# Performance work log

Hardware: AMD Instinct MI355X
Metric: run time of the kernel (lower is better)

Reference implementation:

```python
import jax, jax.numpy as jnp
import numpy as np

TAU = 2.0
V_TH = 1.0
SG_ALPHA = 4.0  # spikingjelly default sigmoid surrogate alpha
BN_EPS = 1e-5

@jax.custom_vjp
def spike_fn(v):
    return (v >= V_TH).astype(v.dtype)

def _spike_fwd(v):
    return spike_fn(v), v

def _spike_bwd(v, g):
    s = jax.nn.sigmoid(SG_ALPHA * (v - V_TH))
    return (g * SG_ALPHA * s * (1.0 - s),)

spike_fn.defvjp(_spike_fwd, _spike_bwd)

def lif(x):
    """Multi-step LIF, tau=2, hard reset to 0, detach_reset. x: (T, ...)."""
    def step(v, xt):
        v = v + (xt - v) / TAU
        s = spike_fn(v)
        v = v * (1.0 - jax.lax.stop_gradient(s))
        return v, s
    _, spikes = jax.lax.scan(step, jnp.zeros_like(x[0]), x)
    return spikes

def batchnorm1d(x, gamma, beta):
    """Training-mode BatchNorm1d over channel dim. x: (N, C, L)."""
    mean = jnp.mean(x, axis=(0, 2), keepdims=True)
    var = jnp.var(x, axis=(0, 2), keepdims=True)  # biased, as torch uses for normalization
    xhat = (x - mean) * jax.lax.rsqrt(var + BN_EPS)
    return xhat * gamma[None, :, None] + beta[None, :, None]

def setup_inputs() -> dict:
    key = jax.random.key(0)
    k_x, k_w1, k_w2 = jax.random.split(key, 3)
    T, B, L, D, H = 4, 64, 64, 768, 3072
    x = jax.random.normal(k_x, (T, B, L, D), dtype=jnp.float32)
    W1 = jax.random.normal(k_w1, (H, D), dtype=jnp.float32) / np.sqrt(D)
    gamma1 = jnp.ones((H,), dtype=jnp.float32)
    beta1 = jnp.zeros((H,), dtype=jnp.float32)
    W2 = jax.random.normal(k_w2, (D, H), dtype=jnp.float32) / np.sqrt(H)
    gamma2 = jnp.ones((D,), dtype=jnp.float32)
    beta2 = jnp.zeros((D,), dtype=jnp.float32)
    return {"x": x, "W1": W1, "gamma1": gamma1, "beta1": beta1,
            "W2": W2, "gamma2": gamma2, "beta2": beta2}

def reference(x, W1, gamma1, beta1, W2, gamma2, beta2):
    T, B, L, D = x.shape
    H = W1.shape[0]
    # --- block 1 ---
    s = lif(x)                                        # (T,B,L,D)
    h = jnp.einsum('tbld,hd->tblh', s, W1)            # (T,B,L,H)
    h = batchnorm1d(h.reshape(T * B, L, H).transpose(0, 2, 1), gamma1, beta1)  # (T*B,H,L)
    # faithful quirk: reshape WITHOUT transposing back
    h = h.reshape(T, B, L, H)
    # --- block 2 ---
    s2 = lif(h)                                       # (T,B,L,H)
    o = jnp.einsum('tblh,dh->tbld', s2, W2)           # (T,B,L,D)
    o = batchnorm1d(o.reshape(T * B, L, D).transpose(0, 2, 1), gamma2, beta2)  # (T*B,D,L)
    o = o.reshape(T, B, L, D)
    return o
```

## Files before the change

kernel.cpp:

```cpp
#include <hip/hip_runtime.h>
#include <stdint.h>
#include <stddef.h>

#define T_ 4
#define B_ 64
#define L_ 64
#define D_ 768
#define H_ 3072
#define M1_ 16384
#define BLD_ 3145728
#define NW_ 2359296
#define HL_ 196608

using f4    = __attribute__((ext_vector_type(4))) float;
using int4v = __attribute__((ext_vector_type(4))) int;
using uc4   = __attribute__((ext_vector_type(4))) unsigned char;
using uc16  = __attribute__((ext_vector_type(16))) unsigned char;
using ui2   = __attribute__((ext_vector_type(2))) unsigned int;

static __device__ __forceinline__ void gload_lds16(const void* g, void* l) {
  __builtin_amdgcn_global_load_lds((const __attribute__((address_space(1))) void*)g,
                                   (__attribute__((address_space(3))) void*)l, 16, 0, 0);
}

#define INV33 (1.0/8589934592.0)

__global__ __launch_bounds__(256) void k_convert(
    const float* __restrict__ W1, const float* __restrict__ W2,
    signed char* __restrict__ Q0, signed char* __restrict__ Q1,
    signed char* __restrict__ Q2, signed char* __restrict__ Q3,
    int* __restrict__ Qint,
    signed char* __restrict__ R0, signed char* __restrict__ R1) {
  int i = blockIdx.x * 256 + threadIdx.x;
  if (i >= NW_) return;
  {
    double w = (double)W1[i];
    long long q = llrint(w * 8589934592.0);
    if (q >  2113929216LL) q =  2113929216LL;
    if (q < -2113929216LL) q = -2113929216LL;
    int ii = (int)q;
    Qint[i] = ii;
    int b0 = ((ii + 128) & 255) - 128; ii = (ii - b0) >> 8;
    int b1 = ((ii + 128) & 255) - 128; ii = (ii - b1) >> 8;
    int b2 = ((ii + 128) & 255) - 128; ii = (ii - b2) >> 8;
    Q0[i] = (signed char)b0; Q1[i] = (signed char)b1;
    Q2[i] = (signed char)b2; Q3[i] = (signed char)ii;
  }
  {
    double w = (double)W2[i];
    long long q = llrint(w * 131072.0);
    if (q >  32512LL) q =  32512LL;
    if (q < -32512LL) q = -32512LL;
    int ii = (int)q;
    int b0 = ((ii + 128) & 255) - 128;
    R0[i] = (signed char)b0;
    R1[i] = (signed char)((ii - b0) >> 8);
  }
}

__global__ __launch_bounds__(256) void k_lif1(const float* __restrict__ x,
                                              unsigned char* __restrict__ s1) {
  size_t i = ((size_t)blockIdx.x * 256 + threadIdx.x) * 4;
  double v0 = 0., v1 = 0., v2 = 0., v3 = 0.;
  #pragma unroll
  for (int t = 0; t < T_; ++t) {
    f4 xt = *(const f4*)(x + (size_t)t * BLD_ + i);
    v0 = v0 + ((double)xt.x - v0) * 0.5;
    v1 = v1 + ((double)xt.y - v1) * 0.5;
    v2 = v2 + ((double)xt.z - v2) * 0.5;
    v3 = v3 + ((double)xt.w - v3) * 0.5;
    uc4 s;
    s.x = (v0 >= 1.0) ? 1 : 0;
    s.y = (v1 >= 1.0) ? 1 : 0;
    s.z = (v2 >= 1.0) ? 1 : 0;
    s.w = (v3 >= 1.0) ? 1 : 0;
    *(uc4*)(s1 + (size_t)t * BLD_ + i) = s;
    v0 = s.x ? 0. : v0;
    v1 = s.y ? 0. : v1;
    v2 = s.z ? 0. : v2;
    v3 = s.w ? 0. : v3;
  }
}

__global__ __launch_bounds__(256) void k_s1t(const unsigned char* __restrict__ s1,
                                             unsigned char* __restrict__ sT,
                                             int* __restrict__ colsum) {
  __shared__ __align__(16) unsigned char sm[64 * 80];
  const int tid = threadIdx.x;
  const int d0 = blockIdx.x * 64;
  const int bl0 = blockIdx.y * 64;
  const int t = blockIdx.z;
  {
    const int i = tid >> 2, ch = tid & 3;
    uc16 v = *(const uc16*)(s1 + (size_t)t * BLD_ + (size_t)(bl0 + i) * 768 + d0 + ch * 16);
    *(uc16*)(sm + i * 80 + ch * 16) = v;
  }
  __syncthreads();
  {
    const int d = tid >> 2, oc = tid & 3;
    union { uc16 v; unsigned char b[16]; } u;
    int s = 0;
    #pragma unroll
    for (int jj = 0; jj < 16; ++jj) {
      unsigned char c = sm[(oc * 16 + jj) * 80 + d];
      u.b[jj] = c;
      s += c;
    }
    *(uc16*)(sT + (size_t)(d0 + d) * M1_ + t * 4096 + bl0 + oc * 16) = u.v;
    s += __shfl_xor(s, 1);
    s += __shfl_xor(s, 2);
    if ((tid & 3) == 0) atomicAdd(&colsum[d0 + d], s);
  }
}

__global__ __launch_bounds__(256, 2) void k_gram(const unsigned char* __restrict__ sT,
                                                 int* __restrict__ Gpart) {
  __shared__ __align__(16) char smem[32768];
  const int tid = threadIdx.x;
  const int lane = tid & 63;
  const int wr = tid >> 7;
  const int wc = (tid >> 6) & 1;
  const int tr = blockIdx.x / 6, tc = blockIdx.x % 6;
  const int ks = blockIdx.y;
  const size_t m0 = (size_t)ks * 2048;

  const int s0 = tid, s1i = tid + 256;
  const int rA0 = s0 >> 2, rA1 = s1i >> 2;
  const int cA0 = (s0 & 3) ^ ((rA0 >> 1) & 3);
  const int cA1 = (s1i & 3) ^ ((rA1 >> 1) & 3);
  const unsigned char* Ag0 = sT + (size_t)(tr * 128 + rA0) * M1_ + m0 + cA0 * 16;
  const unsigned char* Ag1 = sT + (size_t)(tr * 128 + rA1) * M1_ + m0 + cA1 * 16;
  const unsigned char* Bg0 = sT + (size_t)(tc * 128 + rA0) * M1_ + m0 + cA0 * 16;
  const unsigned char* Bg1 = sT + (size_t)(tc * 128 + rA1) * M1_ + m0 + cA1 * 16;

  int4v acc[4][4] = {};
  const int clog = lane >> 4;

  gload_lds16(Ag0, smem + s0 * 16);
  gload_lds16(Ag1, smem + s1i * 16);
  gload_lds16(Bg0, smem + 8192 + s0 * 16);
  gload_lds16(Bg1, smem + 8192 + s1i * 16);
  __syncthreads();

  for (int kt = 0; kt < 32; ++kt) {
    if (kt < 31) {
      const int kn = (kt + 1) * 64;
      char* dst = smem + ((kt + 1) & 1) * 16384;
      gload_lds16(Ag0 + kn, dst + s0 * 16);
      gload_lds16(Ag1 + kn, dst + s1i * 16);
      gload_lds16(Bg0 + kn, dst + 8192 + s0 * 16);
      gload_lds16(Bg1 + kn, dst + 8192 + s1i * 16);
    }
    const signed char* ldsA = (const signed char*)smem + (kt & 1) * 16384;
    const signed char* ldsB = ldsA + 8192;
    int4v av[4], bv[4];
    #pragma unroll
    for (int m = 0; m < 4; ++m) {
      const int r = wr * 64 + m * 16 + (lane & 15);
      const int cp = clog ^ ((r >> 1) & 3);
      av[m] = *(const int4v*)(ldsA + r * 64 + cp * 16);
    }
    #pragma unroll
    for (int n = 0; n < 4; ++n) {
      const int r = wc * 64 + n * 16 + (lane & 15);
      const int cp = clog ^ ((r >> 1) & 3);
      bv[n] = *(const int4v*)(ldsB + r * 64 + cp * 16);
    }
    #pragma unroll
    for (int m = 0; m < 4; ++m)
      #pragma unroll
      for (int n = 0; n < 4; ++n)
        acc[m][n] = __builtin_amdgcn_mfma_i32_16x16x64_i8(av[m], bv[n], acc[m][n], 0, 0, 0);
    __syncthreads();
  }

  const int r0 = tr * 128 + wr * 64 + (clog << 2);
  const int c0 = tc * 128 + wc * 64 + (lane & 15);
  #pragma unroll
  for (int m = 0; m < 4; ++m)
    #pragma unroll
    for (int n = 0; n < 4; ++n)
      #pragma unroll
      for (int rr = 0; rr < 4; ++rr)
        Gpart[((size_t)ks * 768 + r0 + m * 16 + rr) * 768 + c0 + n * 16] = acc[m][n][rr];
}

__global__ __launch_bounds__(256) void k_gramred(const int* __restrict__ Gpart,
                                                 signed char* __restrict__ g0,
                                                 signed char* __restrict__ g1) {
  int i = blockIdx.x * 256 + threadIdx.x;
  if (i >= 768 * 768) return;
  int G = 0;
  #pragma unroll
  for (int ks = 0; ks < 8; ++ks) G += Gpart[(size_t)ks * 768 * 768 + i];
  int b0 = ((G + 128) & 255) - 128;
  g0[i] = (signed char)b0;
  g1[i] = (signed char)((G - b0) >> 8);
}

__global__ __launch_bounds__(256, 2) void k_gq(
    const signed char* __restrict__ g0, const signed char* __restrict__ g1,
    const signed char* __restrict__ Q0, const signed char* __restrict__ Q1,
    const signed char* __restrict__ Q2, const signed char* __restrict__ Q3,
    double* __restrict__ YT) {
  __shared__ __align__(16) char smem[49152];
  const int tid = threadIdx.x;
  const int lane = tid & 63;
  const int w = tid >> 6;
  const int k0 = blockIdx.x * 64;
  const int c0 = blockIdx.y * 64;

  const int row = tid >> 2;
  const int ch = (tid & 3) ^ ((row >> 1) & 3);
  const signed char* Ag[2] = { g0 + (size_t)(k0 + row) * 768 + ch * 16,
                               g1 + (size_t)(k0 + row) * 768 + ch * 16 };
  const signed char* Bg[4] = { Q0 + (size_t)(c0 + row) * 768 + ch * 16,
                               Q1 + (size_t)(c0 + row) * 768 + ch * 16,
                               Q2 + (size_t)(c0 + row) * 768 + ch * 16,
                               Q3 + (size_t)(c0 + row) * 768 + ch * 16 };

  int4v acc[8][4] = {};
  const int clog = lane >> 4;

  #pragma unroll
  for (int a = 0; a < 2; ++a) gload_lds16(Ag[a], smem + a * 4096 + tid * 16);
  #pragma unroll
  for (int p = 0; p < 4; ++p) gload_lds16(Bg[p], smem + 8192 + p * 4096 + tid * 16);
  __syncthreads();

  for (int kt = 0; kt < 12; ++kt) {
    if (kt < 11) {
      const int kn = (kt + 1) * 64;
      char* dst = smem + ((kt + 1) & 1) * 24576;
      #pragma unroll
      for (int a = 0; a < 2; ++a) gload_lds16(Ag[a] + kn, dst + a * 4096 + tid * 16);
      #pragma unroll
      for (int p = 0; p < 4; ++p) gload_lds16(Bg[p] + kn, dst + 8192 + p * 4096 + tid * 16);
    }
    const signed char* base = (const signed char*)smem + (kt & 1) * 24576;
    const int ar = w * 16 + (lane & 15);
    const int acp = clog ^ ((ar >> 1) & 3);
    int4v av[2];
    #pragma unroll
    for (int a = 0; a < 2; ++a)
      av[a] = *(const int4v*)(base + a * 4096 + ar * 64 + acp * 16);
    #pragma unroll
    for (int p = 0; p < 4; ++p) {
      int4v bv[4];
      #pragma unroll
      for (int n = 0; n < 4; ++n) {
        const int br = n * 16 + (lane & 15);
        const int bcp = clog ^ ((br >> 1) & 3);
        bv[n] = *(const int4v*)(base + 8192 + p * 4096 + br * 64 + bcp * 16);
      }
      #pragma unroll
      for (int a = 0; a < 2; ++a)
        #pragma unroll
        for (int n = 0; n < 4; ++n)
          acc[a * 4 + p][n] = __builtin_amdgcn_mfma_i32_16x16x64_i8(av[a], bv[n], acc[a * 4 + p][n], 0, 0, 0);
    }
    __syncthreads();
  }

  #pragma unroll
  for (int n = 0; n < 4; ++n)
    #pragma unroll
    for (int r = 0; r < 4; ++r) {
      int A0 = acc[0][n][r] + (acc[4][n][r] << 8);
      int A1 = acc[1][n][r] + (acc[5][n][r] << 8);
      int A2 = acc[2][n][r] + (acc[6][n][r] << 8);
      int A3 = acc[3][n][r] + (acc[7][n][r] << 8);
      double Y = (double)A0 + 256.0 * (double)A1 + 65536.0 * (double)A2 + 16777216.0 * (double)A3;
      const int k = k0 + w * 16 + clog * 4 + r;
      const int c = c0 + n * 16 + (lane & 15);
      YT[(size_t)c * 768 + k] = Y;
    }
}

__global__ __launch_bounds__(256) void k_stats1(
    const double* __restrict__ YT, const int* __restrict__ Qint,
    const int* __restrict__ colsum,
    double* __restrict__ mean, double* __restrict__ rstd) {
  __shared__ double red[8];
  const int c = blockIdx.x;
  const int tid = threadIdx.x;
  double s2 = 0.0, sm = 0.0;
  for (int k = tid; k < 768; k += 256) {
    double q = (double)Qint[(size_t)c * 768 + k];
    s2 += q * YT[(size_t)c * 768 + k];
    sm += q * (double)colsum[k];
  }
  #pragma unroll
  for (int o = 32; o; o >>= 1) { s2 += __shfl_xor(s2, o); sm += __shfl_xor(sm, o); }
  if ((tid & 63) == 0) { red[(tid >> 6) * 2] = s2; red[(tid >> 6) * 2 + 1] = sm; }
  __syncthreads();
  if (tid == 0) {
    double S2 = red[0] + red[2] + red[4] + red[6];
    double SM = red[1] + red[3] + red[5] + red[7];
    double mn = SM * INV33 * (1.0 / 16384.0);
    double Eh2 = S2 * INV33 * INV33 * (1.0 / 16384.0);
    double var = Eh2 - mn * mn;
    mean[c] = mn;
    rstd[c] = 1.0 / sqrt(var + 1e-5);
  }
}

__global__ __launch_bounds__(256, 2) void k_bnlif(
    const unsigned char* __restrict__ A,
    const signed char* __restrict__ Q0, const signed char* __restrict__ Q1,
    const signed char* __restrict__ Q2, const signed char* __restrict__ Q3,
    const double* __restrict__ mean, const double* __restrict__ rstd,
    const float* __restrict__ gamma, const float* __restrict__ beta,
    signed char* __restrict__ s2) {
  __shared__ __align__(16) char smem[49152];
  const int tid  = threadIdx.x;
  const int lane = tid & 63;
  const int w    = tid >> 6;
  const int wr = tid >> 7;
  const int wc = (tid >> 6) & 1;
  const int n0 = blockIdx.x * 64;
  const int by = blockIdx.y;

  auto grow = [&](int r) -> size_t {
    return (size_t)4096 * (r >> 5) + (size_t)by * 32 + (r & 31);
  };
  const int aIdx0 = w * 128 + lane;
  const int aIdx1 = aIdx0 + 64;
  const int ar0 = aIdx0 >> 2, ar1 = aIdx1 >> 2;
  const int ac0 = (aIdx0 & 3) ^ ((ar0 >> 1) & 3);
  const int ac1 = (aIdx1 & 3) ^ ((ar1 >> 1) & 3);
  const unsigned char* Ag0 = A + grow(ar0) * 768 + ac0 * 16;
  const unsigned char* Ag1 = A + grow(ar1) * 768 + ac1 * 16;
  const int bIdx = w * 64 + lane;
  const int brS = bIdx >> 2;
  const int bcS = (bIdx & 3) ^ ((brS >> 1) & 3);
  const signed char* Bg[4] = { Q0 + (size_t)(n0 + brS) * 768 + bcS * 16,
                               Q1 + (size_t)(n0 + brS) * 768 + bcS * 16,
                               Q2 + (size_t)(n0 + brS) * 768 + bcS * 16,
                               Q3 + (size_t)(n0 + brS) * 768 + bcS * 16 };

  int4v acc[4][4][2] = {};
  const int arow = wr * 64 + (lane & 15);
  const int clog = lane >> 4;

  gload_lds16(Ag0, smem + aIdx0 * 16);
  gload_lds16(Ag1, smem + aIdx1 * 16);
  #pragma unroll
  for (int p = 0; p < 4; ++p) gload_lds16(Bg[p], smem + 8192 + p * 4096 + bIdx * 16);
  __syncthreads();

  for (int kt = 0; kt < 12; ++kt) {
    if (kt < 11) {
      const int kn = (kt + 1) * 64;
      char* dst = smem + ((kt + 1) & 1) * 24576;
      gload_lds16(Ag0 + kn, dst + aIdx0 * 16);
      gload_lds16(Ag1 + kn, dst + aIdx1 * 16);
      #pragma unroll
      for (int p = 0; p < 4; ++p) gload_lds16(Bg[p] + kn, dst + 8192 + p * 4096 + bIdx * 16);
    }
    const signed char* ldsA = (const signed char*)smem + (kt & 1) * 24576;
    const signed char* ldsB = ldsA + 8192;
    int4v av[4], bv[2][4];
    #pragma unroll
    for (int m = 0; m < 4; ++m) {
      const int r = arow + m * 16;
      const int cp = clog ^ ((r >> 1) & 3);
      av[m] = *(const int4v*)(ldsA + r * 64 + cp * 16);
    }
    #pragma unroll
    for (int n = 0; n < 2; ++n) {
      const int r = wc * 32 + n * 16 + (lane & 15);
      const int cp = clog ^ ((r >> 1) & 3);
      #pragma unroll
      for (int p = 0; p < 4; ++p)
        bv[n][p] = *(const int4v*)(ldsB + p * 4096 + r * 64 + cp * 16);
    }
    #pragma unroll
    for (int p = 0; p < 4; ++p)
      #pragma unroll
      for (int m = 0; m < 4; ++m)
        #pragma unroll
        for (int n = 0; n < 2; ++n)
          acc[p][m][n] = __builtin_amdgcn_mfma_i32_16x16x64_i8(av[m], bv[n][p], acc[p][m][n], 0, 0, 0);
    __syncthreads();
  }

  unsigned int* smLo = (unsigned int*)smem;
  short*        smHi = (short*)(smem + 32768);
  #pragma unroll
  for (int m = 0; m < 4; ++m)
    #pragma unroll
    for (int n = 0; n < 2; ++n)
      #pragma unroll
      for (int r = 0; r < 4; ++r) {
        long long h = ((long long)acc[3][m][n][r] << 24) + ((long long)acc[2][m][n][r] << 16)
                    + ((long long)acc[1][m][n][r] << 8) + (long long)acc[0][m][n][r];
        const int rw = wr * 64 + m * 16 + clog * 4 + r;
        const int cl = wc * 32 + n * 16 + (lane & 15);
        smLo[rw * 64 + cl] = (unsigned int)h;
        smHi[rw * 64 + cl] = (short)(h >> 32);
      }
  __syncthreads();

  const int col = tid & 63;
  const int jgrp = tid >> 6;
  const int c = n0 + col;
  const double mn = mean[c], rs = rstd[c];
  const double gm = (double)gamma[c], bt = (double)beta[c];
  const int bI = by >> 1;
  const int l0 = (by & 1) * 32;
  unsigned int plo[4] = {0, 0, 0, 0}, phi[4] = {0, 0, 0, 0};
  #pragma unroll
  for (int jj = 0; jj < 8; ++jj) {
    const int j = jgrp * 8 + jj;
    double v = 0.;
    #pragma unroll
    for (int t = 0; t < 4; ++t) {
      const int rw = t * 32 + j;
      long long h = ((long long)smHi[rw * 64 + col] << 32) | (unsigned long long)smLo[rw * 64 + col];
      double g = ((double)h * INV33 - mn) * rs * gm + bt;
      v = v + (g - v) * 0.5;
      bool s = (v >= 1.0);
      if (s) { if (jj < 4) plo[t] |= 1u << (8 * jj); else phi[t] |= 1u << (8 * (jj - 4)); }
      v = s ? 0. : v;
    }
  }
  #pragma unroll
  for (int t = 0; t < 4; ++t) {
    ui2 wv; wv.x = plo[t]; wv.y = phi[t];
    *(ui2*)(s2 + (size_t)(t * 64 + bI) * HL_ + (size_t)c * 64 + l0 + jgrp * 8) = wv;
  }
}

__global__ __launch_bounds__(256, 2) void k_gemm2(
    const signed char* __restrict__ A,
    const signed char* __restrict__ R0, const signed char* __restrict__ R1,
    float* __restrict__ C,
    double* __restrict__ partS, double* __restrict__ partQ) {
  __shared__ __align__(16) char smem[49152];
  const int tid  = threadIdx.x;
  const int lane = tid & 63;
  const int w    = tid >> 6;
  const int wr = tid >> 7;
  const int wc = (tid >> 6) & 1;
  const int n0 = blockIdx.x * 128;
  const int by = blockIdx.y;

  const int i0 = w * 128 + lane;
  const int i1 = i0 + 64;
  const int r0s = i0 >> 2, r1s = i1 >> 2;
  const int c0s = (i0 & 3) ^ ((r0s >> 1) & 3);
  const int c1s = (i1 & 3) ^ ((r1s >> 1) & 3);
  const signed char* Ag0 = A + (size_t)(by * 128 + r0s) * 3072 + c0s * 16;
  const signed char* Ag1 = A + (size_t)(by * 128 + r1s) * 3072 + c1s * 16;
  const signed char* P0g0 = R0 + (size_t)(n0 + r0s) * 3072 + c0s * 16;
  const signed char* P0g1 = R0 + (size_t)(n0 + r1s) * 3072 + c1s * 16;
  const signed char* P1g0 = R1 + (size_t)(n0 + r0s) * 3072 + c0s * 16;
  const signed char* P1g1 = R1 + (size_t)(n0 + r1s) * 3072 + c1s * 16;

  int4v acc[2][4][4] = {};
  const int arow = wr * 64 + (lane & 15);
  const int brow = wc * 64 + (lane & 15);
  const int clog = lane >> 4;

  gload_lds16(Ag0, smem + i0 * 16);
  gload_lds16(Ag1, smem + i1 * 16);
  gload_lds16(P0g0, smem + 8192 + i0 * 16);
  gload_lds16(P0g1, smem + 8192 + i1 * 16);
  gload_lds16(P1g0, smem + 16384 + i0 * 16);
  gload_lds16(P1g1, smem + 16384 + i1 * 16);
  __syncthreads();

  for (int kt = 0; kt < 48; ++kt) {
    if (kt < 47) {
      const int kn = (kt + 1) * 64;
      char* dst = smem + ((kt + 1) & 1) * 24576;
      gload_lds16(Ag0 + kn, dst + i0 * 16);
      gload_lds16(Ag1 + kn, dst + i1 * 16);
      gload_lds16(P0g0 + kn, dst + 8192 + i0 * 16);
      gload_lds16(P0g1 + kn, dst + 8192 + i1 * 16);
      gload_lds16(P1g0 + kn, dst + 16384 + i0 * 16);
      gload_lds16(P1g1 + kn, dst + 16384 + i1 * 16);
    }
    const signed char* ldsA = (const signed char*)smem + (kt & 1) * 24576;
    int4v av[4], bv[2][4];
    #pragma unroll
    for (int m = 0; m < 4; ++m) {
      const int r = arow + m * 16;
      const int cp = clog ^ ((r >> 1) & 3);
      av[m] = *(const int4v*)(ldsA + r * 64 + cp * 16);
    }
    #pragma unroll
    for (int n = 0; n < 4; ++n) {
      const int r = brow + n * 16;
      const int cp = clog ^ ((r >> 1) & 3);
      bv[0][n] = *(const int4v*)(ldsA + 8192 + r * 64 + cp * 16);
      bv[1][n] = *(const int4v*)(ldsA + 16384 + r * 64 + cp * 16);
    }
    #pragma unroll
    for (int p = 0; p < 2; ++p)
      #pragma unroll
      for (int m = 0; m < 4; ++m)
        #pragma unroll
        for (int n = 0; n < 4; ++n)
          acc[p][m][n] = __builtin_amdgcn_mfma_i32_16x16x64_i8(av[m], bv[p][n], acc[p][m][n], 0, 0, 0);
    __syncthreads();
  }

  const int r0o = by * 128 + wr * 64 + (clog << 2);
  const int c0o = n0 + wc * 64 + (lane & 15);
  #pragma unroll
  for (int n = 0; n < 4; ++n) {
    double s = 0.0, q = 0.0;
    #pragma unroll
    for (int m = 0; m < 4; ++m)
      #pragma unroll
      for (int r = 0; r < 4; ++r) {
        int hv = acc[0][m][n][r] + 256 * acc[1][m][n][r];
        double h = (double)hv * (1.0 / 131072.0);
        C[(size_t)(r0o + m * 16 + r) * 768 + (c0o + n * 16)] = (float)h;
        s += h;
        q += h * h;
      }
    s += __shfl_xor(s, 16);
    q += __shfl_xor(q, 16);
    s += __shfl_xor(s, 32);
    q += __shfl_xor(q, 32);
    if (clog == 0) {
      int col = n0 + wc * 64 + n * 16 + lane;
      partS[(size_t)(by * 2 + wr) * D_ + col] = s;
      partQ[(size_t)(by * 2 + wr) * D_ + col] = q;
    }
  }
}

__global__ __launch_bounds__(256) void k_bnred(
    const double* __restrict__ pS, const double* __restrict__ pQ,
    double* __restrict__ mean, double* __restrict__ rstd, int N, double invM) {
  int i = blockIdx.x * 256 + threadIdx.x;
  if (i >= N) return;
  double s = 0.0, q = 0.0;
  for (int p = 0; p < 256; ++p) {
    s += pS[(size_t)p * N + i];
    q += pQ[(size_t)p * N + i];
  }
  double m = s * invM;
  double v = q * invM - m * m;
  mean[i] = m;
  rstd[i] = 1.0 / sqrt(v + 1e-5);
}

__global__ __launch_bounds__(256) void k_bn2apply(
    const float* __restrict__ O, const double* __restrict__ mean,
    const double* __restrict__ rstd, const float* __restrict__ gamma,
    const float* __restrict__ beta, float* __restrict__ out) {
  __shared__ __align__(16) float sm[64 * 65];
  const int tid = threadIdx.x;
  const int d0 = blockIdx.x * 64;
  const int tb = blockIdx.y;
  const int doff = tid & 63;
  const int lgrp = tid >> 6;
  const double mn = mean[d0 + doff];
  const double rs = rstd[d0 + doff];
  const double gm = (double)gamma[d0 + doff];
  const double bt = (double)beta[d0 + doff];
  #pragma unroll 4
  for (int p = 0; p < 16; ++p) {
    const int l = p * 4 + lgrp;
    double v = (double)O[((size_t)tb * 64 + l) * D_ + d0 + doff];
    sm[doff * 65 + l] = (float)(((v - mn) * rs) * gm + bt);
  }
  __syncthreads();
  const int l4 = (tid & 15) * 4;
  const int db = tid >> 4;
  #pragma unroll
  for (int p = 0; p < 4; ++p) {
    const int dd = p * 16 + db;
    f4 wv;
    wv.x = sm[dd * 65 + l4 + 0];
    wv.y = sm[dd * 65 + l4 + 1];
    wv.z = sm[dd * 65 + l4 + 2];
    wv.w = sm[dd * 65 + l4 + 3];
    *(f4*)(out + (size_t)tb * (D_ * L_) + (size_t)(d0 + dd) * 64 + l4) = wv;
  }
}

extern "C" void kernel_launch(void* const* d_in, const int* in_sizes, int n_in,
                              void* d_out, int out_size, void* d_ws, size_t ws_size,
                              hipStream_t stream) {
  const float* x      = (const float*)d_in[0];
  const float* W1     = (const float*)d_in[1];
  const float* gamma1 = (const float*)d_in[2];
  const float* beta1  = (const float*)d_in[3];
  const float* W2     = (const float*)d_in[4];
  const float* gamma2 = (const float*)d_in[5];
  const float* beta2  = (const float*)d_in[6];
  float* out = (float*)d_out;
  (void)in_sizes; (void)n_in; (void)out_size; (void)ws_size;

  unsigned char* s1 = (unsigned char*)d_out;

  char* ws = (char*)d_ws;
  size_t off = 0;
  auto alloc = [&](size_t bytes) -> void* {
    void* p = ws + off;
    off += (bytes + 255) & ~(size_t)255;
    return p;
  };
  signed char* Q0 = (signed char*)alloc(NW_);
  signed char* Q1 = (signed char*)alloc(NW_);
  signed char* Q2 = (signed char*)alloc(NW_);
  signed char* Q3 = (signed char*)alloc(NW_);
  int* Qint       = (int*)alloc((size_t)NW_ * 4);
  signed char* R0 = (signed char*)alloc(NW_);
  signed char* R1 = (signed char*)alloc(NW_);
  unsigned char* s1T = (unsigned char*)alloc((size_t)768 * M1_);
  int* Gpart      = (int*)alloc((size_t)8 * 768 * 768 * 4);
  signed char* g0 = (signed char*)alloc((size_t)768 * 768);
  signed char* g1 = (signed char*)alloc((size_t)768 * 768);
  double* YT      = (double*)alloc((size_t)H_ * 768 * 8);
  int* colsum     = (int*)alloc(768 * 4);
  signed char* s2 = (signed char*)alloc((size_t)M1_ * H_);
  float* O2       = (float*)alloc((size_t)M1_ * D_ * 4);
  double* pS2 = (double*)alloc((size_t)256 * D_ * 8);
  double* pQ2 = (double*)alloc((size_t)256 * D_ * 8);
  double* mean1 = (double*)alloc((size_t)H_ * 8);
  double* rstd1 = (double*)alloc((size_t)H_ * 8);
  double* mean2 = (double*)alloc((size_t)D_ * 8);
  double* rstd2 = (double*)alloc((size_t)D_ * 8);

  hipMemsetAsync(colsum, 0, 768 * 4, stream);
  k_convert<<<NW_ / 256, 256, 0, stream>>>(W1, W2, Q0, Q1, Q2, Q3, Qint, R0, R1);
  k_lif1<<<BLD_ / 4 / 256, 256, 0, stream>>>(x, s1);
  k_s1t<<<dim3(12, 64, 4), 256, 0, stream>>>(s1, s1T, colsum);
  k_gram<<<dim3(36, 8), 256, 0, stream>>>(s1T, Gpart);
  k_gramred<<<(768 * 768) / 256, 256, 0, stream>>>(Gpart, g0, g1);
  k_gq<<<dim3(12, 48), 256, 0, stream>>>(g0, g1, Q0, Q1, Q2, Q3, YT);
  k_stats1<<<H_, 256, 0, stream>>>(YT, Qint, colsum, mean1, rstd1);
  k_bnlif<<<dim3(H_ / 64, (B_ * L_) / 32), 256, 0, stream>>>(
      s1, Q0, Q1, Q2, Q3, mean1, rstd1, gamma1, beta1, s2);
  k_gemm2<<<dim3(D_ / 128, M1_ / 128), 256, 0, stream>>>(s2, R0, R1, O2, pS2, pQ2);
  k_bnred<<<(D_ + 255) / 256, 256, 0, stream>>>(pS2, pQ2, mean2, rstd2, D_, 1.0 / (double)M1_);
  k_bn2apply<<<dim3(D_ / 64, T_ * B_), 256, 0, stream>>>(O2, mean2, rstd2, gamma2, beta2, out);
}
```

Baseline: 404.4 us.

## Triple-buffer LDS in both int8 GEMM kernels with explicit vmcnt waits

Both int8 MFMA GEMM kernels move from double-buffered to triple-buffered LDS staging. Loads are issued two k-tiles ahead, and partial s_waitcnt vmcnt counts let the loop wait only for the tile about to be consumed instead of draining every load. Raw s_barrier calls with sched_barrier fences replace __syncthreads. The goal is to hide global-load latency behind MFMA work, at the cost of LDS growing from 48 KB to 72 KB per block, which may cut occupancy under launch_bounds(256,2).

After: 380.5 us, median of 2. -5.9%, faster.

```diff
diff --git a/kernel.cpp b/kernel.cpp
--- a/kernel.cpp
+++ b/kernel.cpp
@@ -22,6 +22,9 @@
   __builtin_amdgcn_global_load_lds((const __attribute__((address_space(1))) void*)g,
                                    (__attribute__((address_space(3))) void*)l, 16, 0, 0);
 }
+
+#define SGB() __builtin_amdgcn_sched_barrier(0)
+#define HWBAR() __builtin_amdgcn_s_barrier()
 
 #define INV33 (1.0/8589934592.0)
 
@@ -312,7 +315,7 @@
     const double* __restrict__ mean, const double* __restrict__ rstd,
     const float* __restrict__ gamma, const float* __restrict__ beta,
     signed char* __restrict__ s2) {
-  __shared__ __align__(16) char smem[49152];
+  __shared__ __align__(16) char smem[73728];
   const int tid  = threadIdx.x;
   const int lane = tid & 63;
   const int w    = tid >> 6;
@@ -343,22 +346,26 @@
   const int arow = wr * 64 + (lane & 15);
   const int clog = lane >> 4;
 
-  gload_lds16(Ag0, smem + aIdx0 * 16);
-  gload_lds16(Ag1, smem + aIdx1 * 16);
-  #pragma unroll
-  for (int p = 0; p < 4; ++p) gload_lds16(Bg[p], smem + 8192 + p * 4096 + bIdx * 16);
-  __syncthreads();
-
+  auto stage = [&](int t) {
+    char* dst = smem + (t % 3) * 24576;
+    const int kn = t * 64;
+    gload_lds16(Ag0 + kn, dst + aIdx0 * 16);
+    gload_lds16(Ag1 + kn, dst + aIdx1 * 16);
+    #pragma unroll
+    for (int p = 0; p < 4; ++p) gload_lds16(Bg[p] + kn, dst + 8192 + p * 4096 + bIdx * 16);
+  };
+
+  stage(0);
+  stage(1);
   for (int kt = 0; kt < 12; ++kt) {
-    if (kt < 11) {
-      const int kn = (kt + 1) * 64;
-      char* dst = smem + ((kt + 1) & 1) * 24576;
-      gload_lds16(Ag0 + kn, dst + aIdx0 * 16);
-      gload_lds16(Ag1 + kn, dst + aIdx1 * 16);
-      #pragma unroll
-      for (int p = 0; p < 4; ++p) gload_lds16(Bg[p] + kn, dst + 8192 + p * 4096 + bIdx * 16);
-    }
-    const signed char* ldsA = (const signed char*)smem + (kt & 1) * 24576;
+    if (kt <= 9) stage(kt + 2);
+    if (kt <= 9)       { asm volatile("s_waitcnt vmcnt(12)" ::: "memory"); }
+    else if (kt == 10) { asm volatile("s_waitcnt vmcnt(6)" ::: "memory"); }
+    else               { asm volatile("s_waitcnt vmcnt(0)" ::: "memory"); }
+    SGB();
+    HWBAR();
+    SGB();
+    const signed char* ldsA = (const signed char*)smem + (kt % 3) * 24576;
     const signed char* ldsB = ldsA + 8192;
     int4v av[4], bv[2][4];
     #pragma unroll
@@ -382,7 +389,8 @@
         #pragma unroll
         for (int n = 0; n < 2; ++n)
           acc[p][m][n] = __builtin_amdgcn_mfma_i32_16x16x64_i8(av[m], bv[n][p], acc[p][m][n], 0, 0, 0);
-    __syncthreads();
+    SGB();
+    HWBAR();
   }
 
   unsigned int* smLo = (unsigned int*)smem;
@@ -437,7 +445,7 @@
     const signed char* __restrict__ R0, const signed char* __restrict__ R1,
     float* __restrict__ C,
     double* __restrict__ partS, double* __restrict__ partQ) {
-  __shared__ __align__(16) char smem[49152];
+  __shared__ __align__(16) char smem[73728];
   const int tid  = threadIdx.x;
   const int lane = tid & 63;
   const int w    = tid >> 6;
@@ -463,26 +471,28 @@
   const int brow = wc * 64 + (lane & 15);
   const int clog = lane >> 4;
 
-  gload_lds16(Ag0, smem + i0 * 16);
-  gload_lds16(Ag1, smem + i1 * 16);
-  gload_lds16(P0g0, smem + 8192 + i0 * 16);
-  gload_lds16(P0g1, smem + 8192 + i1 * 16);
-  gload_lds16(P1g0, smem + 16384 + i0 * 16);
-  gload_lds16(P1g1, smem + 16384 + i1 * 16);
-  __syncthreads();
-
+  auto stage = [&](int t) {
+    char* dst = smem + (t % 3) * 24576;
+    const int kn = t * 64;
+    gload_lds16(Ag0 + kn, dst + i0 * 16);
+    gload_lds16(Ag1 + kn, dst + i1 * 16);
+    gload_lds16(P0g0 + kn, dst + 8192 + i0 * 16);
+    gload_lds16(P0g1 + kn, dst + 8192 + i1 * 16);
+    gload_lds16(P1g0 + kn, dst + 16384 + i0 * 16);
+    gload_lds16(P1g1 + kn, dst + 16384 + i1 * 16);
+  };
+
+  stage(0);
+  stage(1);
   for (int kt = 0; kt < 48; ++kt) {
-    if (kt < 47) {
-      const int kn = (kt + 1) * 64;
-      char* dst = smem + ((kt + 1) & 1) * 24576;
-      gload_lds16(Ag0 + kn, dst + i0 * 16);
-      gload_lds16(Ag1 + kn, dst + i1 * 16);
-      gload_lds16(P0g0 + kn, dst + 8192 + i0 * 16);
-      gload_lds16(P0g1 + kn, dst + 8192 + i1 * 16);
-      gload_lds16(P1g0 + kn, dst + 16384 + i0 * 16);
-      gload_lds16(P1g1 + kn, dst + 16384 + i1 * 16);
-    }
-    const signed char* ldsA = (const signed char*)smem + (kt & 1) * 24576;
+    if (kt <= 45) stage(kt + 2);
+    if (kt <= 45)      { asm volatile("s_waitcnt vmcnt(12)" ::: "memory"); }
+    else if (kt == 46) { asm volatile("s_waitcnt vmcnt(6)" ::: "memory"); }
+    else               { asm volatile("s_waitcnt vmcnt(0)" ::: "memory"); }
+    SGB();
+    HWBAR();
+    SGB();
+    const signed char* ldsA = (const signed char*)smem + (kt % 3) * 24576;
     int4v av[4], bv[2][4];
     #pragma unroll
     for (int m = 0; m < 4; ++m) {
@@ -504,7 +514,8 @@
         #pragma unroll
         for (int n = 0; n < 4; ++n)
           acc[p][m][n] = __builtin_amdgcn_mfma_i32_16x16x64_i8(av[m], bv[p][n], acc[p][m][n], 0, 0, 0);
-    __syncthreads();
+    SGB();
+    HWBAR();
   }
 
   const int r0o = by * 128 + wr * 64 + (clog << 2);
```
